# Kernel tuning notes

Measured on AMD Instinct MI355X. Metric: run time of the kernel, lower is better.

The kernel has to match this reference:

```python
import jax, jax.numpy as jnp
import numpy as np

N_NODES = 100000
N_EDGES = 3200000
F_IN = 128
F_HID = 16
F_OUT = 1


def setup_inputs() -> dict:
    key = jax.random.key(0)
    ks = jax.random.split(key, 8)
    x = jax.random.normal(ks[0], (N_NODES, F_IN), dtype=jnp.float32)
    src = jax.random.randint(ks[1], (N_EDGES,), 0, N_NODES, dtype=jnp.int32)
    dst = jax.random.randint(ks[2], (N_EDGES,), 0, N_NODES, dtype=jnp.int32)
    edge_w = jax.random.uniform(ks[3], (N_EDGES,), dtype=jnp.float32)
    W0 = jax.random.normal(ks[4], (F_IN, F_HID), dtype=jnp.float32) / np.sqrt(F_IN)
    b0 = jnp.zeros((F_HID,), dtype=jnp.float32)
    W1 = jax.random.normal(ks[5], (F_HID, F_OUT), dtype=jnp.float32) / np.sqrt(F_HID)
    b1 = jnp.zeros((F_OUT,), dtype=jnp.float32)
    return {"x": x, "src": src, "dst": dst, "edge_w": edge_w,
            "W0": W0, "b0": b0, "W1": W1, "b1": b1}


def _spmm(src, dst, edge_w, h):
    # sparse A (COO) @ dense h: gather rows at src, weight, scatter-add to dst
    msgs = h[src] * edge_w[:, None]            # [E, F]
    return jax.ops.segment_sum(msgs, dst, num_segments=N_NODES)  # [N, F]


def reference(x, src, dst, edge_w, W0, b0, W1, b1):
    # GCNConv layer 0: relu(A @ (x @ W0) + b0)
    z0 = x @ W0                                 # [N, 16] linear transform first
    h = jax.nn.relu(_spmm(src, dst, edge_w, z0) + b0)
    # (Dropout is identity at inference)
    # GCNConv layer 1: sigmoid(A @ (h @ W1) + b1)
    z1 = h @ W1                                 # [N, 1]
    out = jax.nn.sigmoid(_spmm(src, dst, edge_w, z1) + b1)
    return out
```

## Files before the change

kernel.cpp:

```cpp
#include <hip/hip_runtime.h>

#define N_NODES 100000
#define N_EDGES 3200000
#define F_IN 128
#define F_HID 16

#define BK_LG 7
#define BK_NODES 128
#define NB ((N_NODES + BK_NODES - 1) / BK_NODES)
#define NB_P 1024
#define BCAP 4800
#define CHUNK 4096
#define BIN_T 512
#define EPT (CHUNK / BIN_T)
#define CUR_STRIDE 16

__device__ __forceinline__ unsigned short f2bf_rne(float f) {
    unsigned u = __float_as_uint(f);
    u += 0x7FFFu + ((u >> 16) & 1u);
    return (unsigned short)(u >> 16);
}

__global__ __launch_bounds__(256) void k_xw0(const float* __restrict__ x,
                                             const float* __restrict__ W0,
                                             unsigned short* __restrict__ z0b, int n) {
    __shared__ float xs[64][F_IN + 1];
    __shared__ float w0s[F_IN * F_HID];
    const int tid = threadIdx.x;
    for (int i = tid; i < F_IN * F_HID; i += 256) w0s[i] = W0[i];
    const int row0 = blockIdx.x * 64;
    for (int i = tid; i < 64 * (F_IN / 4); i += 256) {
        int r  = i / (F_IN / 4);
        int c4 = i % (F_IN / 4);
        float4 v = make_float4(0.f, 0.f, 0.f, 0.f);
        int row = row0 + r;
        if (row < n) v = ((const float4*)(x + (size_t)row * F_IN))[c4];
        xs[r][c4 * 4 + 0] = v.x; xs[r][c4 * 4 + 1] = v.y;
        xs[r][c4 * 4 + 2] = v.z; xs[r][c4 * 4 + 3] = v.w;
    }
    __syncthreads();
    const int r  = tid & 63;
    const int cg = tid >> 6;
    float a0 = 0.f, a1 = 0.f, a2 = 0.f, a3 = 0.f;
    #pragma unroll 8
    for (int k = 0; k < F_IN; ++k) {
        float xv = xs[r][k];
        a0 = fmaf(xv, w0s[k * F_HID + cg * 4 + 0], a0);
        a1 = fmaf(xv, w0s[k * F_HID + cg * 4 + 1], a1);
        a2 = fmaf(xv, w0s[k * F_HID + cg * 4 + 2], a2);
        a3 = fmaf(xv, w0s[k * F_HID + cg * 4 + 3], a3);
    }
    int row = row0 + r;
    if (row < n) {
        ushort4 p = make_ushort4(f2bf_rne(a0), f2bf_rne(a1), f2bf_rne(a2), f2bf_rne(a3));
        *(ushort4*)(z0b + (size_t)row * F_HID + cg * 4) = p;
    }
}

__global__ __launch_bounds__(BIN_T) void k_bin(const int* __restrict__ src,
                                               const int* __restrict__ dst,
                                               const float* __restrict__ ew,
                                               int* __restrict__ gcursor,
                                               int2* __restrict__ ebin) {
    __shared__ int cnt[NB_P], excl[NB_P], run[NB_P], gb[NB_P], alw[NB_P];
    __shared__ int2 stage[CHUNK];
    __shared__ unsigned short sbid[CHUNK];
    __shared__ int wsum[8];
    const int tid  = threadIdx.x;
    const int lane = tid & 63, wid = tid >> 6;
    const int e0   = blockIdx.x * CHUNK;
    const int nch  = min(CHUNK, N_EDGES - e0);

    for (int i = tid; i < NB_P; i += BIN_T) cnt[i] = 0;
    __syncthreads();

    int es[EPT], eb[EPT], edl[EPT]; float ww[EPT];
    #pragma unroll
    for (int k = 0; k < EPT; ++k) {
        int idx = k * BIN_T + tid;
        if (idx < nch) {
            int e = e0 + idx;
            int d = dst[e];
            es[k]  = src[e];
            ww[k]  = ew[e];
            eb[k]  = d >> BK_LG;
            edl[k] = d & (BK_NODES - 1);
            atomicAdd(&cnt[eb[k]], 1);
        } else {
            eb[k] = -1;
        }
    }
    __syncthreads();

    {
        int c0 = cnt[2 * tid], c1 = cnt[2 * tid + 1];
        int s  = c0 + c1;
        int sc = s;
        #pragma unroll
        for (int off = 1; off < 64; off <<= 1) {
            int t = __shfl_up(sc, off);
            if (lane >= off) sc += t;
        }
        if (lane == 63) wsum[wid] = sc;
        __syncthreads();
        if (wid == 0 && lane < 8) {
            int wv = wsum[lane];
            #pragma unroll
            for (int off = 1; off < 8; off <<= 1) {
                int t = __shfl_up(wv, off);
                if (lane >= off) wv += t;
            }
            wsum[lane] = wv;
        }
        __syncthreads();
        int base = (wid > 0 ? wsum[wid - 1] : 0) + (sc - s);
        excl[2 * tid]     = base;
        excl[2 * tid + 1] = base + c0;
    }
    __syncthreads();

    for (int b = tid; b < NB; b += BIN_T) {
        int c = cnt[b];
        if (c > 0) {
            int old = atomicAdd(&gcursor[b * CUR_STRIDE], c);
            int a = BCAP - old;
            a = (a < 0) ? 0 : ((a > c) ? c : a);
            alw[b] = a;
            gb[b]  = b * BCAP + old;
        } else {
            alw[b] = 0;
            gb[b]  = b * BCAP;
        }
        run[b] = 0;
    }
    __syncthreads();

    #pragma unroll
    for (int k = 0; k < EPT; ++k) {
        if (eb[k] >= 0) {
            int b = eb[k];
            int p = excl[b] + atomicAdd(&run[b], 1);
            stage[p] = make_int2(__float_as_int(ww[k]), es[k] | (edl[k] << 17));
            sbid[p]  = (unsigned short)b;
        }
    }
    __syncthreads();

    for (int s = tid; s < nch; s += BIN_T) {
        int b   = sbid[s];
        int off = s - excl[b];
        if (off < alw[b]) ebin[(size_t)gb[b] + off] = stage[s];
    }
}

__global__ __launch_bounds__(512) void k_sg0(const int* __restrict__ gcursor,
                                             const int2* __restrict__ ebin,
                                             const unsigned short* __restrict__ z0b,
                                             const float* __restrict__ b0,
                                             const float* __restrict__ W1,
                                             float* __restrict__ z1) {
    __shared__ int2 stage[BCAP];
    __shared__ unsigned short idx[BCAP];
    __shared__ int hist[BK_NODES], scn[BK_NODES], run[BK_NODES];
    __shared__ float b0s[16], w1s[16];
    const int tid  = threadIdx.x;
    const int lane = tid & 63, wid = tid >> 6;
    const int b    = blockIdx.x;
    if (tid < 16)        { b0s[tid] = b0[tid]; w1s[tid] = W1[tid]; }
    if (tid < BK_NODES)  hist[tid] = 0;
    __syncthreads();

    const int   ecnt = min(gcursor[b * CUR_STRIDE], BCAP);
    const int2* eb   = ebin + (size_t)b * BCAP;
    for (int i = tid; i < ecnt; i += 512) {
        int2 e = eb[i];
        stage[i] = e;
        atomicAdd(&hist[e.y >> 17], 1);
    }
    __syncthreads();

    if (tid < BK_NODES) scn[tid] = hist[tid];
    __syncthreads();
    for (int off = 1; off < BK_NODES; off <<= 1) {
        int v = 0;
        if (tid < BK_NODES && tid >= off) v = scn[tid - off];
        __syncthreads();
        if (tid < BK_NODES && tid >= off) scn[tid] += v;
        __syncthreads();
    }
    if (tid < BK_NODES) { int e = scn[tid] - hist[tid]; scn[tid] = e; run[tid] = 0; }
    __syncthreads();

    for (int i = tid; i < ecnt; i += 512) {
        int dl = stage[i].y >> 17;
        int r  = atomicAdd(&run[dl], 1);
        idx[scn[dl] + r] = (unsigned short)i;
    }
    __syncthreads();

    for (int n = wid; n < BK_NODES; n += 8) {
        const int v = b * BK_NODES + n;
        if (v >= N_NODES) continue;
        const int beg = scn[n], dv = hist[n];
        const int f2  = lane & 7;
        const int g   = lane >> 3;
        float acc0 = 0.f, acc1 = 0.f;
        for (int j = g; j < dv; j += 16) {
            int2 e0 = stage[idx[beg + j]];
            int  j1 = j + 8;
            int2 e1 = (j1 < dv) ? stage[idx[beg + j1]] : stage[0];
            if (j1 >= dv) e1.x = 0;
            unsigned u0 = *(const unsigned*)(z0b + (size_t)(e0.y & 0x1FFFF) * F_HID + f2 * 2);
            unsigned u1 = *(const unsigned*)(z0b + (size_t)(e1.y & 0x1FFFF) * F_HID + f2 * 2);
            float w0 = __int_as_float(e0.x), w1 = __int_as_float(e1.x);
            acc0 = fmaf(__uint_as_float(u0 << 16),         w0, acc0);
            acc1 = fmaf(__uint_as_float(u0 & 0xFFFF0000u), w0, acc1);
            acc0 = fmaf(__uint_as_float(u1 << 16),         w1, acc0);
            acc1 = fmaf(__uint_as_float(u1 & 0xFFFF0000u), w1, acc1);
        }
        acc0 += __shfl_xor(acc0, 8);  acc1 += __shfl_xor(acc1, 8);
        acc0 += __shfl_xor(acc0, 16); acc1 += __shfl_xor(acc1, 16);
        acc0 += __shfl_xor(acc0, 32); acc1 += __shfl_xor(acc1, 32);
        float c = fmaxf(acc0 + b0s[f2 * 2], 0.f) * w1s[f2 * 2]
                + fmaxf(acc1 + b0s[f2 * 2 + 1], 0.f) * w1s[f2 * 2 + 1];
        c += __shfl_xor(c, 1);
        c += __shfl_xor(c, 2);
        c += __shfl_xor(c, 4);
        if (lane == 0) z1[v] = c;
    }
}

__global__ __launch_bounds__(256) void k_g1(const int* __restrict__ gcursor,
                                            const int2* __restrict__ ebin,
                                            const float* __restrict__ z1,
                                            const float* __restrict__ b1,
                                            float* __restrict__ out) {
    __shared__ float acc[BK_NODES];
    const int tid = threadIdx.x;
    const int b   = blockIdx.x;
    if (tid < BK_NODES) acc[tid] = 0.f;
    __syncthreads();
    const int   ecnt = min(gcursor[b * CUR_STRIDE], BCAP);
    const int2* eb   = ebin + (size_t)b * BCAP;
    for (int i = tid; i < ecnt; i += 512) {
        int2 e0 = eb[i];
        int  i1 = i + 256;
        int2 e1 = (i1 < ecnt) ? eb[i1] : make_int2(0, 0);
        float m0 = z1[e0.y & 0x1FFFF] * __int_as_float(e0.x);
        float m1 = z1[e1.y & 0x1FFFF] * __int_as_float(e1.x);
        atomicAdd(&acc[e0.y >> 17], m0);
        if (i1 < ecnt) atomicAdd(&acc[e1.y >> 17], m1);
    }
    __syncthreads();
    if (tid < BK_NODES) {
        int v = b * BK_NODES + tid;
        if (v < N_NODES) out[v] = 1.f / (1.f + expf(-(acc[tid] + b1[0])));
    }
}

extern "C" void kernel_launch(void* const* d_in, const int* in_sizes, int n_in,
                              void* d_out, int out_size, void* d_ws, size_t ws_size,
                              hipStream_t stream) {
    const float* x   = (const float*)d_in[0];
    const int*   src = (const int*)d_in[1];
    const int*   dst = (const int*)d_in[2];
    const float* ew  = (const float*)d_in[3];
    const float* W0  = (const float*)d_in[4];
    const float* b0  = (const float*)d_in[5];
    const float* W1  = (const float*)d_in[6];
    const float* b1  = (const float*)d_in[7];
    float* out = (float*)d_out;

    unsigned short* z0b = (unsigned short*)d_ws;
    float* z1      = (float*)(z0b + (size_t)N_NODES * F_HID);
    int*   gcursor = (int*)(z1 + N_NODES);
    int2*  ebin    = (int2*)(gcursor + NB * CUR_STRIDE);

    hipMemsetAsync(gcursor, 0, (size_t)NB * CUR_STRIDE * sizeof(int), stream);

    k_bin <<<(N_EDGES + CHUNK - 1) / CHUNK, BIN_T, 0, stream>>>(src, dst, ew,
                                                                gcursor, ebin);
    k_xw0 <<<(N_NODES + 63) / 64, 256, 0, stream>>>(x, W0, z0b, N_NODES);
    k_sg0 <<<NB, 512, 0, stream>>>(gcursor, ebin, z0b, b0, W1, z1);
    k_g1  <<<NB, 256, 0, stream>>>(gcursor, ebin, z1, b1, out);
}
```

Measured before the change: 149.1 us.

## Split edge binning into two-pass radix scatter via coarse 1024-node buckets

Replaces the single-pass scatter of edges into 782 fine buckets with two passes: first into 98 coarse buckets of 1024 nodes, then each coarse bucket is split into 8 fine buckets. Each pass writes to far fewer destinations per chunk, so global writes should be more contiguous and the per-block shared histogram and scan are smaller. The cost is an extra kernel launch plus another full read and write of the 3.2M packed edges. Coarse capacity limits could silently drop edges if the degree distribution were skewed.

```diff
diff --git a/kernel.cpp b/kernel.cpp
--- a/kernel.cpp
+++ b/kernel.cpp
@@ -8,8 +8,13 @@
 #define BK_LG 7
 #define BK_NODES 128
 #define NB ((N_NODES + BK_NODES - 1) / BK_NODES)
-#define NB_P 1024
-#define BCAP 4800
+#define BCAPF 4800
+#define CLG 10
+#define CNODES 1024
+#define NBC ((N_NODES + CNODES - 1) / CNODES)
+#define NBC_P 128
+#define BCAPC 34816
+#define CPB2 9
 #define CHUNK 4096
 #define BIN_T 512
 #define EPT (CHUNK / BIN_T)
@@ -57,21 +62,19 @@
     }
 }
 
-__global__ __launch_bounds__(BIN_T) void k_bin(const int* __restrict__ src,
-                                               const int* __restrict__ dst,
-                                               const float* __restrict__ ew,
-                                               int* __restrict__ gcursor,
-                                               int2* __restrict__ ebin) {
-    __shared__ int cnt[NB_P], excl[NB_P], run[NB_P], gb[NB_P], alw[NB_P];
+__global__ __launch_bounds__(BIN_T) void k_bin1(const int* __restrict__ src,
+                                                const int* __restrict__ dst,
+                                                const float* __restrict__ ew,
+                                                int* __restrict__ cursorC,
+                                                int2* __restrict__ ebinC) {
+    __shared__ int cnt[NBC_P], excl[NBC_P], run[NBC_P], gb[NBC_P], alw[NBC_P];
     __shared__ int2 stage[CHUNK];
-    __shared__ unsigned short sbid[CHUNK];
-    __shared__ int wsum[8];
-    const int tid  = threadIdx.x;
-    const int lane = tid & 63, wid = tid >> 6;
-    const int e0   = blockIdx.x * CHUNK;
-    const int nch  = min(CHUNK, N_EDGES - e0);
-
-    for (int i = tid; i < NB_P; i += BIN_T) cnt[i] = 0;
+    __shared__ unsigned char sbid[CHUNK];
+    const int tid = threadIdx.x;
+    const int e0  = blockIdx.x * CHUNK;
+    const int nch = min(CHUNK, N_EDGES - e0);
+
+    for (int i = tid; i < NBC_P; i += BIN_T) cnt[i] = 0;
     __syncthreads();
 
     int es[EPT], eb[EPT], edl[EPT]; float ww[EPT];
@@ -83,8 +86,8 @@
             int d = dst[e];
             es[k]  = src[e];
             ww[k]  = ew[e];
-            eb[k]  = d >> BK_LG;
-            edl[k] = d & (BK_NODES - 1);
+            eb[k]  = d >> CLG;
+            edl[k] = d & (CNODES - 1);
             atomicAdd(&cnt[eb[k]], 1);
         } else {
             eb[k] = -1;
@@ -92,46 +95,31 @@
     }
     __syncthreads();
 
-    {
-        int c0 = cnt[2 * tid], c1 = cnt[2 * tid + 1];
-        int s  = c0 + c1;
-        int sc = s;
-        #pragma unroll
-        for (int off = 1; off < 64; off <<= 1) {
-            int t = __shfl_up(sc, off);
-            if (lane >= off) sc += t;
-        }
-        if (lane == 63) wsum[wid] = sc;
+    if (tid < NBC_P) excl[tid] = cnt[tid];
+    __syncthreads();
+    for (int off = 1; off < NBC_P; off <<= 1) {
+        int v = 0;
+        if (tid < NBC_P && tid >= off) v = excl[tid - off];
         __syncthreads();
-        if (wid == 0 && lane < 8) {
-            int wv = wsum[lane];
-            #pragma unroll
-            for (int off = 1; off < 8; off <<= 1) {
-                int t = __shfl_up(wv, off);
-                if (lane >= off) wv += t;
-            }
-            wsum[lane] = wv;
-        }
+        if (tid < NBC_P && tid >= off) excl[tid] += v;
         __syncthreads();
-        int base = (wid > 0 ? wsum[wid - 1] : 0) + (sc - s);
-        excl[2 * tid]     = base;
-        excl[2 * tid + 1] = base + c0;
-    }
-    __syncthreads();
-
-    for (int b = tid; b < NB; b += BIN_T) {
-        int c = cnt[b];
+    }
+    if (tid < NBC_P) excl[tid] -= cnt[tid];
+    __syncthreads();
+
+    if (tid < NBC) {
+        int c = cnt[tid];
         if (c > 0) {
-            int old = atomicAdd(&gcursor[b * CUR_STRIDE], c);
-            int a = BCAP - old;
+            int old = atomicAdd(&cursorC[tid * CUR_STRIDE], c);
+            int a = BCAPC - old;
             a = (a < 0) ? 0 : ((a > c) ? c : a);
-            alw[b] = a;
-            gb[b]  = b * BCAP + old;
+            alw[tid] = a;
+            gb[tid]  = tid * BCAPC + old;
         } else {
-            alw[b] = 0;
-            gb[b]  = b * BCAP;
-        }
-        run[b] = 0;
+            alw[tid] = 0;
+            gb[tid]  = tid * BCAPC;
+        }
+        run[tid] = 0;
     }
     __syncthreads();
 
@@ -141,7 +129,7 @@
             int b = eb[k];
             int p = excl[b] + atomicAdd(&run[b], 1);
             stage[p] = make_int2(__float_as_int(ww[k]), es[k] | (edl[k] << 17));
-            sbid[p]  = (unsigned short)b;
+            sbid[p]  = (unsigned char)b;
         }
     }
     __syncthreads();
@@ -149,29 +137,118 @@
     for (int s = tid; s < nch; s += BIN_T) {
         int b   = sbid[s];
         int off = s - excl[b];
-        if (off < alw[b]) ebin[(size_t)gb[b] + off] = stage[s];
-    }
-}
-
-__global__ __launch_bounds__(512) void k_sg0(const int* __restrict__ gcursor,
-                                             const int2* __restrict__ ebin,
+        if (off < alw[b]) ebinC[(size_t)gb[b] + off] = stage[s];
+    }
+}
+
+__global__ __launch_bounds__(BIN_T) void k_bin2(const int* __restrict__ cursorC,
+                                                const int2* __restrict__ ebinC,
+                                                int* __restrict__ cursorF,
+                                                int2* __restrict__ ebinF) {
+    __shared__ int cntw[64], runw[64], base[64];
+    __shared__ int totals[8], excl_s[8], gb8[8], alw8[8];
+    __shared__ int2 stage[CHUNK];
+    __shared__ unsigned char sbid[CHUNK];
+    const int tid = threadIdx.x;
+    const int wid = tid >> 6;
+    const int c   = blockIdx.x / CPB2;
+    const int ck  = blockIdx.x % CPB2;
+    const int ecnt = min(cursorC[c * CUR_STRIDE], BCAPC);
+    const int beg  = ck * CHUNK;
+    const int n2   = min(CHUNK, ecnt - beg);
+    if (n2 <= 0) return;
+    const int2* eC = ebinC + (size_t)c * BCAPC + beg;
+
+    if (tid < 64) { cntw[tid] = 0; runw[tid] = 0; }
+    __syncthreads();
+
+    int fid[EPT]; int2 pk[EPT];
+    #pragma unroll
+    for (int k = 0; k < EPT; ++k) {
+        int idx = k * BIN_T + tid;
+        if (idx < n2) {
+            int2 e = eC[idx];
+            int dlc = e.y >> 17;
+            int f   = dlc >> BK_LG;
+            fid[k]  = f;
+            pk[k]   = make_int2(e.x, (e.y & 0x1FFFF) | ((dlc & (BK_NODES - 1)) << 17));
+            atomicAdd(&cntw[f * 8 + wid], 1);
+        } else {
+            fid[k] = -1;
+        }
+    }
+    __syncthreads();
+
+    if (tid < 8) {
+        int t = 0;
+        #pragma unroll
+        for (int w = 0; w < 8; ++w) t += cntw[tid * 8 + w];
+        totals[tid] = t;
+    }
+    __syncthreads();
+    if (tid < 8) {
+        int e = 0;
+        for (int f = 0; f < 8; ++f) if (f < tid) e += totals[f];
+        excl_s[tid] = e;
+        int t = totals[tid];
+        int fb = c * 8 + tid;
+        if (t > 0 && fb < NB) {
+            int old = atomicAdd(&cursorF[fb * CUR_STRIDE], t);
+            int a = BCAPF - old;
+            a = (a < 0) ? 0 : ((a > t) ? t : a);
+            alw8[tid] = a;
+            gb8[tid]  = fb * BCAPF + old;
+        } else {
+            alw8[tid] = 0;
+            gb8[tid]  = 0;
+        }
+    }
+    __syncthreads();
+    if (tid < 64) {
+        int f = tid >> 3, w = tid & 7;
+        int bb = excl_s[f];
+        for (int w2 = 0; w2 < 8; ++w2) if (w2 < w) bb += cntw[f * 8 + w2];
+        base[tid] = bb;
+    }
+    __syncthreads();
+
+    #pragma unroll
+    for (int k = 0; k < EPT; ++k) {
+        if (fid[k] >= 0) {
+            int slot = fid[k] * 8 + wid;
+            int p = base[slot] + atomicAdd(&runw[slot], 1);
+            stage[p] = pk[k];
+            sbid[p]  = (unsigned char)fid[k];
+        }
+    }
+    __syncthreads();
+
+    for (int s = tid; s < n2; s += BIN_T) {
+        int f   = sbid[s];
+        int off = s - excl_s[f];
+        if (off < alw8[f]) ebinF[(size_t)gb8[f] + off] = stage[s];
+    }
+}
+
+__global__ __launch_bounds__(512) void k_sg0(const int* __restrict__ cursorF,
+                                             const int2* __restrict__ ebinF,
                                              const unsigned short* __restrict__ z0b,
                                              const float* __restrict__ b0,
                                              const float* __restrict__ W1,
                                              float* __restrict__ z1) {
-    __shared__ int2 stage[BCAP];
-    __shared__ unsigned short idx[BCAP];
+    __shared__ int2 stage[BCAPF];
+    __shared__ unsigned short idx[BCAPF];
     __shared__ int hist[BK_NODES], scn[BK_NODES], run[BK_NODES];
     __shared__ float b0s[16], w1s[16];
     const int tid  = threadIdx.x;
     const int lane = tid & 63, wid = tid >> 6;
     const int b    = blockIdx.x;
-    if (tid < 16)        { b0s[tid] = b0[tid]; w1s[tid] = W1[tid]; }
-    if (tid < BK_NODES)  hist[tid] = 0;
-    __syncthreads();
-
-    const int   ecnt = min(gcursor[b * CUR_STRIDE], BCAP);
-    const int2* eb   = ebin + (size_t)b * BCAP;
+    if (tid < 16)       { b0s[tid] = b0[tid]; w1s[tid] = W1[tid]; }
+    if (tid < BK_NODES) hist[tid] = 0;
+    __syncthreads();
+
+    const int   ecnt = min(cursorF[b * CUR_STRIDE], BCAPF);
+    const int2* eb   = ebinF + (size_t)b * BCAPF;
     for (int i = tid; i < ecnt; i += 512) {
         int2 e = eb[i];
         stage[i] = e;
@@ -221,17 +298,17 @@
         acc0 += __shfl_xor(acc0, 8);  acc1 += __shfl_xor(acc1, 8);
         acc0 += __shfl_xor(acc0, 16); acc1 += __shfl_xor(acc1, 16);
         acc0 += __shfl_xor(acc0, 32); acc1 += __shfl_xor(acc1, 32);
-        float c = fmaxf(acc0 + b0s[f2 * 2], 0.f) * w1s[f2 * 2]
-                + fmaxf(acc1 + b0s[f2 * 2 + 1], 0.f) * w1s[f2 * 2 + 1];
-        c += __shfl_xor(c, 1);
-        c += __shfl_xor(c, 2);
-        c += __shfl_xor(c, 4);
-        if (lane == 0) z1[v] = c;
-    }
-}
-
-__global__ __launch_bounds__(256) void k_g1(const int* __restrict__ gcursor,
-                                            const int2* __restrict__ ebin,
+        float cc = fmaxf(acc0 + b0s[f2 * 2], 0.f) * w1s[f2 * 2]
+                 + fmaxf(acc1 + b0s[f2 * 2 + 1], 0.f) * w1s[f2 * 2 + 1];
+        cc += __shfl_xor(cc, 1);
+        cc += __shfl_xor(cc, 2);
+        cc += __shfl_xor(cc, 4);
+        if (lane == 0) z1[v] = cc;
+    }
+}
+
+__global__ __launch_bounds__(256) void k_g1(const int* __restrict__ cursorF,
+                                            const int2* __restrict__ ebinF,
                                             const float* __restrict__ z1,
                                             const float* __restrict__ b1,
                                             float* __restrict__ out) {
@@ -240,8 +317,8 @@
     const int b   = blockIdx.x;
     if (tid < BK_NODES) acc[tid] = 0.f;
     __syncthreads();
-    const int   ecnt = min(gcursor[b * CUR_STRIDE], BCAP);
-    const int2* eb   = ebin + (size_t)b * BCAP;
+    const int   ecnt = min(cursorF[b * CUR_STRIDE], BCAPF);
+    const int2* eb   = ebinF + (size_t)b * BCAPF;
     for (int i = tid; i < ecnt; i += 512) {
         int2 e0 = eb[i];
         int  i1 = i + 256;
@@ -273,14 +350,18 @@
 
     unsigned short* z0b = (unsigned short*)d_ws;
     float* z1      = (float*)(z0b + (size_t)N_NODES * F_HID);
-    int*   gcursor = (int*)(z1 + N_NODES);
-    int2*  ebin    = (int2*)(gcursor + NB * CUR_STRIDE);
-
-    hipMemsetAsync(gcursor, 0, (size_t)NB * CUR_STRIDE * sizeof(int), stream);
-
-    k_bin <<<(N_EDGES + CHUNK - 1) / CHUNK, BIN_T, 0, stream>>>(src, dst, ew,
-                                                                gcursor, ebin);
+    int*   cursorC = (int*)(z1 + N_NODES);
+    int*   cursorF = cursorC + NBC * CUR_STRIDE;
+    int2*  ebinC   = (int2*)(cursorF + NB * CUR_STRIDE);
+    int2*  ebinF   = ebinC + (size_t)NBC * BCAPC;
+
+    hipMemsetAsync(cursorC, 0,
+                   (size_t)(NBC + NB) * CUR_STRIDE * sizeof(int), stream);
+
+    k_bin1<<<(N_EDGES + CHUNK - 1) / CHUNK, BIN_T, 0, stream>>>(src, dst, ew,
+                                                                cursorC, ebinC);
     k_xw0 <<<(N_NODES + 63) / 64, 256, 0, stream>>>(x, W0, z0b, N_NODES);
-    k_sg0 <<<NB, 512, 0, stream>>>(gcursor, ebin, z0b, b0, W1, z1);
-    k_g1  <<<NB, 256, 0, stream>>>(gcursor, ebin, z1, b1, out);
-}
+    k_bin2<<<NBC * CPB2, BIN_T, 0, stream>>>(cursorC, ebinC, cursorF, ebinF);
+    k_sg0 <<<NB, 512, 0, stream>>>(cursorF, ebinF, z0b, b0, W1, z1);
+    k_g1  <<<NB, 256, 0, stream>>>(cursorF, ebinF, z1, b1, out);
+}
```

After: 148.2 us. About the same (-0.6%).
